# Performance work log

Measured on AMD Instinct MI355X. Metric: run time of the kernel, lower is better.

The kernel has to match this reference:

```python
import jax, jax.numpy as jnp
import numpy as np

K_MAX, K_MIN = 12.0, 1.0
TEMP = 1.0
STE_ALPHA = 12.0
EPS = 1e-8

DIM, HID, KHID, WHID = 512, 2048, 128, 128
B, N = 8, 1024


def setup_inputs() -> dict:
    key = jax.random.key(0)
    ks = jax.random.split(key, 13)
    def lin(k, fan_in, shape):
        bound = 1.0 / np.sqrt(fan_in)
        return jax.random.uniform(k, shape, jnp.float32, -bound, bound)
    return {
        "x": jax.random.normal(ks[0], (B, N, DIM), jnp.float32),
        "fc1_w": lin(ks[1], DIM, (HID, DIM)),
        "fc1_b": lin(ks[2], DIM, (HID,)),
        "fc2_w": lin(ks[3], HID, (DIM, HID)),
        "fc2_b": lin(ks[4], HID, (DIM,)),
        "k1_w": lin(ks[5], DIM, (KHID, DIM)),
        "k1_b": lin(ks[6], DIM, (KHID,)),
        "k2_w": lin(ks[7], KHID, (3, KHID)),
        "k2_b": lin(ks[8], KHID, (3,)),
        "w1_w": lin(ks[9], DIM, (WHID, DIM)),
        "w1_b": lin(ks[10], DIM, (WHID,)),
        "w2_w": lin(ks[11], WHID, (3, WHID)),
        "w2_b": lin(ks[12], WHID, (3,)),
    }


def adaptive_knn_aggregate(h, k_cont):
    # h: (B,N,C), k_cont: (B,) continuous k in [k_min, k_max]
    sim = jnp.einsum("bnc,bmc->bnm", h, h) / TEMP          # (B,N,N)
    order = jnp.argsort(-sim, axis=-1)                      # descending
    rank = jnp.argsort(order, axis=-1).astype(h.dtype)      # rank 0 = most similar
    # soft top-k gate (STE-style sigmoid around k_cont)
    gate = jax.nn.sigmoid(STE_ALPHA * (k_cont[:, None, None] - (rank + 0.5)))
    attn = jax.nn.softmax(sim, axis=-1) * gate
    attn = attn / (attn.sum(axis=-1, keepdims=True) + EPS)
    return jnp.einsum("bnm,bmc->bnc", attn, h)


def reference(x, fc1_w, fc1_b, fc2_w, fc2_b, k1_w, k1_b, k2_w, k2_b,
              w1_w, w1_b, w2_w, w2_b):
    pooled = x.mean(axis=1)                                 # (B,C)
    # adaptive k values net
    kh = jax.nn.relu(pooled @ k1_w.T + k1_b)
    ratio = jax.nn.sigmoid(kh @ k2_w.T + k2_b)              # (B,3)
    k_cont = K_MIN + ratio * (K_MAX - K_MIN)
    # adaptive branch weights net
    wh = jax.nn.relu(pooled @ w1_w.T + w1_b)
    w = jax.nn.softmax(wh @ w2_w.T + w2_b, axis=-1)         # (B,3)
    # MLP (dropout p=0 -> identity)
    h = jax.nn.relu(x @ fc1_w.T + fc1_b)
    h = h @ fc2_w.T + fc2_b                                 # (B,N,C)
    # three KNN aggregation branches blended by w
    y = sum(adaptive_knn_aggregate(h, k_cont[:, i]) * w[:, i, None, None]
            for i in range(3))
    return y
```

## Files before the change

### kernel.cpp

```cpp
#include <hip/hip_runtime.h>
#include <math.h>

#define DIM_ 512
#define HID_ 2048
#define B_ 8
#define N_ 1024
#define ROWS_ 8192
#define TOPK 16

typedef __attribute__((ext_vector_type(8))) short short8;
typedef __attribute__((ext_vector_type(4))) float float4v;

__device__ __forceinline__ float sigm(float x) { return 1.f / (1.f + __expf(-x)); }

__device__ __forceinline__ short f2bf(float f) {
    unsigned u = __float_as_uint(f);
    u += 0x7FFF + ((u >> 16) & 1);
    return (short)(u >> 16);
}

__device__ __forceinline__ float bf2f(unsigned short s) {
    return __uint_as_float((unsigned)s << 16);
}

__device__ __forceinline__ unsigned f2ord(float f) {
    unsigned u = __float_as_uint(f);
    return (u & 0x80000000u) ? ~u : (u | 0x80000000u);
}

__device__ __forceinline__ void gload16(const short* g, short* l) {
    __builtin_amdgcn_global_load_lds(
        (const __attribute__((address_space(1))) void*)g,
        (__attribute__((address_space(3))) void*)l, 16, 0, 0);
}

__global__ __launch_bounds__(256)
void cvt_w_kernel(const float* __restrict__ w1, const float* __restrict__ w2,
                  short* __restrict__ o1, short* __restrict__ o2) {
    const int i = blockIdx.x * 256 + threadIdx.x;
    const int n4 = HID_ * DIM_ / 4;
    const float* in = (i < n4) ? w1 : w2;
    short* out = (i < n4) ? o1 : o2;
    const int j = (i < n4) ? i : (i - n4);
    const float4 v = *(const float4*)(in + (long long)j * 4);
    short4 o;
    o.x = f2bf(v.x); o.y = f2bf(v.y); o.z = f2bf(v.z); o.w = f2bf(v.w);
    *(short4*)(out + (long long)j * 4) = o;
}

__global__ __launch_bounds__(512)
void pool_part_cvt_kernel(const float* __restrict__ x, float* __restrict__ part,
                          short* __restrict__ xb) {
    const int bx = blockIdx.x;
    const int b = bx >> 5, chunk = bx & 31;
    const int c = threadIdx.x;
    const long long base = ((long long)b * N_ + chunk * 32) * DIM_ + c;
    const float* xp = x + base;
    short* xo = xb + base;
    float s = 0.f;
    for (int n = 0; n < 32; ++n) {
        const float v = xp[(long long)n * DIM_];
        s += v;
        xo[(long long)n * DIM_] = f2bf(v);
    }
    part[(long long)bx * DIM_ + c] = s;
}

__global__ __launch_bounds__(512)
void pool_heads_kernel(const float* __restrict__ part,
                       const float* __restrict__ k1w, const float* __restrict__ k1b,
                       const float* __restrict__ k2w, const float* __restrict__ k2b,
                       const float* __restrict__ w1w, const float* __restrict__ w1b,
                       const float* __restrict__ w2w, const float* __restrict__ w2b,
                       float* __restrict__ kcont, float* __restrict__ wbr) {
    const int b = blockIdx.x;
    const int t = threadIdx.x;
    __shared__ float sp[DIM_];
    __shared__ float kh[128], wh[128];
    __shared__ float wraw[4];
    float s = 0.f;
    for (int g = 0; g < 32; ++g) s += part[((long long)b * 32 + g) * DIM_ + t];
    sp[t] = s * (1.f / 1024.f);
    __syncthreads();
    if (t < 128) {
        float ak = k1b[t], aw = w1b[t];
        for (int k = 0; k < DIM_; ++k) {
            const float pv = sp[k];
            ak = fmaf(pv, k1w[t * DIM_ + k], ak);
            aw = fmaf(pv, w1w[t * DIM_ + k], aw);
        }
        kh[t] = fmaxf(ak, 0.f);
        wh[t] = fmaxf(aw, 0.f);
    }
    __syncthreads();
    if (t < 3) {
        float rk = k2b[t], rw = w2b[t];
        for (int k = 0; k < 128; ++k) {
            rk = fmaf(kh[k], k2w[t * 128 + k], rk);
            rw = fmaf(wh[k], w2w[t * 128 + k], rw);
        }
        kcont[b * 3 + t] = 1.f + 11.f * sigm(rk);
        wraw[t] = rw;
    }
    __syncthreads();
    if (t == 0) {
        const float m = fmaxf(wraw[0], fmaxf(wraw[1], wraw[2]));
        const float e0 = __expf(wraw[0] - m), e1 = __expf(wraw[1] - m), e2 = __expf(wraw[2] - m);
        const float inv = 1.f / (e0 + e1 + e2);
        wbr[b * 3 + 0] = e0 * inv;
        wbr[b * 3 + 1] = e1 * inv;
        wbr[b * 3 + 2] = e2 * inv;
    }
}

template<int OUTMODE>
__global__ __launch_bounds__(256)
void gemm_mfma(const short* __restrict__ A, const short* __restrict__ Bm,
               const float* __restrict__ bias,
               float* __restrict__ outF, short* __restrict__ outB,
               int M, int N, int K, int lda, int ldb,
               long long sA, long long sB, long long sC) {
    const int bz = blockIdx.z;
    A  += (long long)bz * sA;
    Bm += (long long)bz * sB;

    __shared__ short As[128 * 64];
    __shared__ short Bs[128 * 64];

    const int tid = threadIdx.x;
    const int lane = tid & 63;
    const int wv = tid >> 6;
    const int m0 = blockIdx.y * 128;
    const int n0 = blockIdx.x * 128;

    const int lrow = lane >> 3;
    const int cg = (lane & 7) ^ lrow;

    const int ml = (wv & 1) * 64;
    const int nl = (wv >> 1) * 64;
    const int fr = lane & 15;
    const int kq = lane >> 4;

    float4v acc[4][4];
#pragma unroll
    for (int i = 0; i < 4; ++i)
#pragma unroll
        for (int j = 0; j < 4; ++j) acc[i][j] = (float4v){0.f, 0.f, 0.f, 0.f};

    for (int k0 = 0; k0 < K; k0 += 64) {
        __syncthreads();
#pragma unroll
        for (int i = 0; i < 4; ++i) {
            const int rloc = wv * 32 + i * 8 + lrow;
            gload16(A + (long long)(m0 + rloc) * lda + (k0 + cg * 8),
                    &As[(wv * 32 + i * 8) * 64]);
            gload16(Bm + (long long)(n0 + rloc) * ldb + (k0 + cg * 8),
                    &Bs[(wv * 32 + i * 8) * 64]);
        }
        __syncthreads();
#pragma unroll
        for (int ks = 0; ks < 2; ++ks) {
            const int c = ks * 4 + kq;
            short8 af[4], bfr[4];
#pragma unroll
            for (int i = 0; i < 4; ++i) {
                const int m = ml + i * 16 + fr;
                af[i] = *(const short8*)&As[m * 64 + ((c ^ (m & 7)) * 8)];
                const int n = nl + i * 16 + fr;
                bfr[i] = *(const short8*)&Bs[n * 64 + ((c ^ (n & 7)) * 8)];
            }
#pragma unroll
            for (int i = 0; i < 4; ++i)
#pragma unroll
                for (int j = 0; j < 4; ++j)
                    acc[i][j] = __builtin_amdgcn_mfma_f32_16x16x32_bf16(
                        af[i], bfr[j], acc[i][j], 0, 0, 0);
        }
    }

    const long long outOfs = (long long)bz * sC;
#pragma unroll
    for (int i = 0; i < 4; ++i) {
#pragma unroll
        for (int j = 0; j < 4; ++j) {
            const int ng = n0 + nl + j * 16 + fr;
            float bv = 0.f;
            if (OUTMODE != 2) bv = bias[ng];
#pragma unroll
            for (int r = 0; r < 4; ++r) {
                const int mg = m0 + ml + i * 16 + kq * 4 + r;
                float v = acc[i][j][r] + bv;
                if (OUTMODE == 0) v = fmaxf(v, 0.f);
                const long long idx = outOfs + (long long)mg * N + ng;
                if (OUTMODE == 2) outF[idx] = v;
                else              outB[idx] = f2bf(v);
            }
        }
    }
}

__global__ __launch_bounds__(256)
void combine_kernel(const float* __restrict__ p0, const float* __restrict__ p1,
                    const float* __restrict__ bias, short* __restrict__ out) {
    const int i = blockIdx.x * 256 + threadIdx.x;
    const long long o = (long long)i * 4;
    const float4 a = *(const float4*)(p0 + o);
    const float4 b = *(const float4*)(p1 + o);
    const int col = (int)(o & (DIM_ - 1));
    const float4 bs = *(const float4*)(bias + col);
    short4 r;
    r.x = f2bf(a.x + b.x + bs.x);
    r.y = f2bf(a.y + b.y + bs.y);
    r.z = f2bf(a.z + b.z + bs.z);
    r.w = f2bf(a.w + b.w + bs.w);
    *(short4*)(out + o) = r;
}

__global__ __launch_bounds__(256)
void topk_agg_kernel(const float* __restrict__ sim,
                     const float* __restrict__ kcont, const float* __restrict__ wbr,
                     const unsigned short* __restrict__ h, float* __restrict__ y) {
    const int wv = threadIdx.x >> 6;
    const int lane = threadIdx.x & 63;
    const int ll = lane & 15;
    const int row = blockIdx.x * 4 + wv;
    const int b = row >> 10;
    const float* srow = sim + (long long)row * N_;

    float f[16];
    const int base = lane * 16;
#pragma unroll
    for (int q = 0; q < 4; ++q) {
        const float4 v = *(const float4*)(srow + base + q * 4);
        f[q * 4 + 0] = v.x; f[q * 4 + 1] = v.y; f[q * 4 + 2] = v.z; f[q * 4 + 3] = v.w;
    }

    float lmax = f[0];
#pragma unroll
    for (int j = 1; j < 16; ++j) lmax = fmaxf(lmax, f[j]);
#pragma unroll
    for (int d = 32; d > 0; d >>= 1) lmax = fmaxf(lmax, __shfl_xor(lmax, d));
    const float maxv = lmax;

    float lsum = 0.f;
#pragma unroll
    for (int j = 0; j < 16; ++j) lsum += __expf(f[j] - maxv);
#pragma unroll
    for (int d = 32; d > 0; d >>= 1) lsum += __shfl_xor(lsum, d);
    const float invden = 1.f / lsum;

    unsigned key[16];
#pragma unroll
    for (int j = 0; j < 16; ++j)
        key[j] = (f2ord(f[j]) & 0xFFFFFC00u) | (unsigned)(1023 - (base + j));

#pragma unroll
    for (int k = 2; k <= 16; k <<= 1) {
#pragma unroll
        for (int j = k >> 1; j > 0; j >>= 1) {
#pragma unroll
            for (int i = 0; i < 16; ++i) {
                const int l = i ^ j;
                if (l > i) {
                    const bool desc = ((i & k) == 0);
                    const unsigned a = key[i], bk = key[l];
                    const unsigned hi = (a > bk) ? a : bk;
                    const unsigned lo = (a > bk) ? bk : a;
                    key[i] = desc ? hi : lo;
                    key[l] = desc ? lo : hi;
                }
            }
        }
    }

#pragma unroll
    for (int d = 1; d < 64; d <<= 1) {
        unsigned other[16];
#pragma unroll
        for (int i = 0; i < 16; ++i)
            other[i] = __shfl_xor(key[15 - i], d);
#pragma unroll
        for (int i = 0; i < 16; ++i)
            key[i] = (key[i] > other[i]) ? key[i] : other[i];
#pragma unroll
        for (int j = 8; j > 0; j >>= 1) {
#pragma unroll
            for (int i = 0; i < 16; ++i) {
                if ((i & j) == 0) {
                    const unsigned a = key[i], bk = key[i | j];
                    key[i]     = (a > bk) ? a : bk;
                    key[i | j] = (a > bk) ? bk : a;
                }
            }
        }
    }

    unsigned k32 = key[0];
#pragma unroll
    for (int j = 1; j < 16; ++j) k32 = (ll == j) ? key[j] : k32;
    const int myidx = 1023 - (int)(k32 & 1023u);
    const float myval = srow[myidx];

    unsigned long long kx = ((unsigned long long)f2ord(myval) << 32)
                          | (unsigned)(1023 - myidx);
#pragma unroll
    for (int k = 2; k <= 16; k <<= 1) {
#pragma unroll
        for (int d = k >> 1; d > 0; d >>= 1) {
            const unsigned long long other = __shfl_xor(kx, d);
            const bool keepMax = (((ll & k) != 0) == ((ll & d) != 0));
            const bool mineBig = (kx > other);
            kx = (keepMax == mineBig) ? kx : other;
        }
    }
    const unsigned sord = (unsigned)(kx >> 32);
    const unsigned su = (sord & 0x80000000u) ? (sord & 0x7FFFFFFFu) : ~sord;
    const float sval = __uint_as_float(su);
    const int sidx = 1023 - (int)(kx & 1023u);

    const float kc0 = kcont[b * 3 + 0], kc1 = kcont[b * 3 + 1], kc2 = kcont[b * 3 + 2];
    const float w0 = wbr[b * 3 + 0], w1 = wbr[b * 3 + 1], w2 = wbr[b * 3 + 2];

    const float p = __expf(sval - maxv) * invden;
    const float rr = (float)ll + 0.5f;
    const float g0 = sigm(12.f * (kc0 - rr));
    const float g1 = sigm(12.f * (kc1 - rr));
    const float g2 = sigm(12.f * (kc2 - rr));
    float s0 = p * g0, s1 = p * g1, s2 = p * g2;
#pragma unroll
    for (int d = 1; d < 16; d <<= 1) {
        s0 += __shfl_xor(s0, d);
        s1 += __shfl_xor(s1, d);
        s2 += __shfl_xor(s2, d);
    }
    const float f0 = w0 / (s0 + 1e-8f);
    const float f1 = w1 / (s1 + 1e-8f);
    const float f2 = w2 / (s2 + 1e-8f);
    const float mycoef = p * (f0 * g0 + f1 * g1 + f2 * g2);

    const int gbase = lane & 48;
    const unsigned short* hbase = h + (long long)b * (N_ * DIM_) + lane * 8;
    float acc[8] = {0.f, 0.f, 0.f, 0.f, 0.f, 0.f, 0.f, 0.f};
#pragma unroll
    for (int r = 0; r < 16; ++r) {
        const float coef = __shfl(mycoef, gbase | r);
        const int idx = __shfl(sidx, gbase | r);
        const ushort4 h0 = *(const ushort4*)(hbase + (long long)idx * DIM_);
        const ushort4 h1 = *(const ushort4*)(hbase + (long long)idx * DIM_ + 4);
        acc[0] = fmaf(coef, bf2f(h0.x), acc[0]);
        acc[1] = fmaf(coef, bf2f(h0.y), acc[1]);
        acc[2] = fmaf(coef, bf2f(h0.z), acc[2]);
        acc[3] = fmaf(coef, bf2f(h0.w), acc[3]);
        acc[4] = fmaf(coef, bf2f(h1.x), acc[4]);
        acc[5] = fmaf(coef, bf2f(h1.y), acc[5]);
        acc[6] = fmaf(coef, bf2f(h1.z), acc[6]);
        acc[7] = fmaf(coef, bf2f(h1.w), acc[7]);
    }
    float* yp = y + (long long)row * DIM_ + lane * 8;
    *(float4*)(yp + 0) = make_float4(acc[0], acc[1], acc[2], acc[3]);
    *(float4*)(yp + 4) = make_float4(acc[4], acc[5], acc[6], acc[7]);
}

extern "C" void kernel_launch(void* const* d_in, const int* in_sizes, int n_in,
                              void* d_out, int out_size, void* d_ws, size_t ws_size,
                              hipStream_t stream) {
    const float* x     = (const float*)d_in[0];
    const float* fc1_w = (const float*)d_in[1];
    const float* fc1_b = (const float*)d_in[2];
    const float* fc2_w = (const float*)d_in[3];
    const float* fc2_b = (const float*)d_in[4];
    const float* k1_w  = (const float*)d_in[5];
    const float* k1_b  = (const float*)d_in[6];
    const float* k2_w  = (const float*)d_in[7];
    const float* k2_b  = (const float*)d_in[8];
    const float* w1_w  = (const float*)d_in[9];
    const float* w1_b  = (const float*)d_in[10];
    const float* w2_w  = (const float*)d_in[11];
    const float* w2_b  = (const float*)d_in[12];

    char* ws = (char*)d_ws;
    short* h1b    = (short*)(ws + 0);
    float* simbuf = (float*)(ws + 0);
    short* xb     = (short*)(ws + 33554432);
    float* part0  = (float*)(ws + 33554432);
    float* part1  = (float*)(ws + 50331648);
    short* hb     = (short*)(ws + 67108864);
    short* w1b    = (short*)(ws + 75497472);
    short* w2b    = (short*)(ws + 77594624);
    float* ppart  = (float*)(ws + 79691776);
    float* kcont  = (float*)(ws + 80216064);
    float* wbr    = (float*)(ws + 80216192);

    float* y = (float*)d_out;

    cvt_w_kernel<<<dim3(2 * HID_ * DIM_ / 4 / 256), dim3(256), 0, stream>>>(fc1_w, fc2_w, w1b, w2b);
    pool_part_cvt_kernel<<<dim3(B_ * 32), dim3(512), 0, stream>>>(x, ppart, xb);
    pool_heads_kernel<<<dim3(B_), dim3(512), 0, stream>>>(ppart, k1_w, k1_b, k2_w, k2_b,
                                                          w1_w, w1_b, w2_w, w2_b, kcont, wbr);
    gemm_mfma<0><<<dim3(HID_ / 128, ROWS_ / 128, 1), dim3(256), 0, stream>>>(
        xb, w1b, fc1_b, nullptr, h1b, ROWS_, HID_, DIM_, DIM_, DIM_, 0, 0, 0);
    gemm_mfma<2><<<dim3(DIM_ / 128, ROWS_ / 128, 2), dim3(256), 0, stream>>>(
        h1b, w2b, nullptr, part0, nullptr, ROWS_, DIM_, HID_ / 2, HID_, HID_,
        (long long)(HID_ / 2), (long long)(HID_ / 2), (long long)ROWS_ * DIM_);
    combine_kernel<<<dim3(ROWS_ * DIM_ / 4 / 256), dim3(256), 0, stream>>>(part0, part1, fc2_b, hb);
    gemm_mfma<2><<<dim3(N_ / 128, N_ / 128, B_), dim3(256), 0, stream>>>(
        hb, hb, nullptr, simbuf, nullptr, N_, N_, DIM_, DIM_, DIM_,
        (long long)N_ * DIM_, (long long)N_ * DIM_, (long long)N_ * N_);
    topk_agg_kernel<<<dim3(ROWS_ / 4), dim3(256), 0, stream>>>(
        simbuf, kcont, wbr, (const unsigned short*)hb, y);
}
```

Measured before the change: 223.9 us.

## Switch GEMM to 32x32x16 MFMA and merge weight/input conversion kernels

The GEMM inner loop moves from 16x16x32 bf16 MFMA tiles (4x4 per wave) to 32x32x16 tiles (2x2 per wave), which halves the LDS fragment reads per MFMA and uses a larger matrix instruction. The epilogue row mapping is rewritten to match the 32x32 accumulator layout. Separately, the weight-conversion kernel and the pooling/x-conversion kernel are merged into one launch, removing one kernel launch. The larger accumulator layout changes the store pattern, so global write coalescing may differ.

```diff
diff --git a/kernel.cpp b/kernel.cpp
--- a/kernel.cpp
+++ b/kernel.cpp
@@ -9,7 +9,7 @@
 #define TOPK 16
 
 typedef __attribute__((ext_vector_type(8))) short short8;
-typedef __attribute__((ext_vector_type(4))) float float4v;
+typedef __attribute__((ext_vector_type(16))) float float16v;
 
 __device__ __forceinline__ float sigm(float x) { return 1.f / (1.f + __expf(-x)); }
 
@@ -34,36 +34,38 @@
         (__attribute__((address_space(3))) void*)l, 16, 0, 0);
 }
 
-__global__ __launch_bounds__(256)
-void cvt_w_kernel(const float* __restrict__ w1, const float* __restrict__ w2,
-                  short* __restrict__ o1, short* __restrict__ o2) {
-    const int i = blockIdx.x * 256 + threadIdx.x;
-    const int n4 = HID_ * DIM_ / 4;
-    const float* in = (i < n4) ? w1 : w2;
-    short* out = (i < n4) ? o1 : o2;
-    const int j = (i < n4) ? i : (i - n4);
-    const float4 v = *(const float4*)(in + (long long)j * 4);
-    short4 o;
-    o.x = f2bf(v.x); o.y = f2bf(v.y); o.z = f2bf(v.z); o.w = f2bf(v.w);
-    *(short4*)(out + (long long)j * 4) = o;
-}
-
 __global__ __launch_bounds__(512)
-void pool_part_cvt_kernel(const float* __restrict__ x, float* __restrict__ part,
-                          short* __restrict__ xb) {
+void prep_kernel(const float* __restrict__ x, float* __restrict__ part, short* __restrict__ xb,
+                 const float* __restrict__ w1, const float* __restrict__ w2,
+                 short* __restrict__ o1, short* __restrict__ o2) {
     const int bx = blockIdx.x;
-    const int b = bx >> 5, chunk = bx & 31;
-    const int c = threadIdx.x;
-    const long long base = ((long long)b * N_ + chunk * 32) * DIM_ + c;
-    const float* xp = x + base;
-    short* xo = xb + base;
-    float s = 0.f;
-    for (int n = 0; n < 32; ++n) {
-        const float v = xp[(long long)n * DIM_];
-        s += v;
-        xo[(long long)n * DIM_] = f2bf(v);
-    }
-    part[(long long)bx * DIM_ + c] = s;
+    if (bx < 256) {
+        const int b = bx >> 5, chunk = bx & 31;
+        const int c = threadIdx.x;
+        const long long base = ((long long)b * N_ + chunk * 32) * DIM_ + c;
+        const float* xp = x + base;
+        short* xo = xb + base;
+        float s = 0.f;
+        for (int n = 0; n < 32; ++n) {
+            const float v = xp[(long long)n * DIM_];
+            s += v;
+            xo[(long long)n * DIM_] = f2bf(v);
+        }
+        part[(long long)bx * DIM_ + c] = s;
+    } else {
+        const int n4 = HID_ * DIM_ / 4;
+        int i = (bx - 256) * 2048 + threadIdx.x;
+#pragma unroll
+        for (int t = 0; t < 4; ++t, i += 512) {
+            const float* in = (i < n4) ? w1 : w2;
+            short* out = (i < n4) ? o1 : o2;
+            const int j = (i < n4) ? i : (i - n4);
+            const float4 v = *(const float4*)(in + (long long)j * 4);
+            short4 o;
+            o.x = f2bf(v.x); o.y = f2bf(v.y); o.z = f2bf(v.z); o.w = f2bf(v.w);
+            *(short4*)(out + (long long)j * 4) = o;
+        }
+    }
 }
 
 __global__ __launch_bounds__(512)
@@ -138,14 +140,16 @@
 
     const int ml = (wv & 1) * 64;
     const int nl = (wv >> 1) * 64;
-    const int fr = lane & 15;
-    const int kq = lane >> 4;
-
-    float4v acc[4][4];
-#pragma unroll
-    for (int i = 0; i < 4; ++i)
-#pragma unroll
-        for (int j = 0; j < 4; ++j) acc[i][j] = (float4v){0.f, 0.f, 0.f, 0.f};
+    const int fr = lane & 31;
+    const int kh = lane >> 5;
+
+    float16v acc[2][2];
+#pragma unroll
+    for (int i = 0; i < 2; ++i)
+#pragma unroll
+        for (int j = 0; j < 2; ++j)
+#pragma unroll
+            for (int r = 0; r < 16; ++r) acc[i][j][r] = 0.f;
 
     for (int k0 = 0; k0 < K; k0 += 64) {
         __syncthreads();
@@ -159,36 +163,36 @@
         }
         __syncthreads();
 #pragma unroll
-        for (int ks = 0; ks < 2; ++ks) {
-            const int c = ks * 4 + kq;
-            short8 af[4], bfr[4];
-#pragma unroll
-            for (int i = 0; i < 4; ++i) {
-                const int m = ml + i * 16 + fr;
-                af[i] = *(const short8*)&As[m * 64 + ((c ^ (m & 7)) * 8)];
-                const int n = nl + i * 16 + fr;
-                bfr[i] = *(const short8*)&Bs[n * 64 + ((c ^ (n & 7)) * 8)];
+        for (int c = 0; c < 4; ++c) {
+            const int ch = c * 2 + kh;
+            short8 af[2], bfr[2];
+#pragma unroll
+            for (int i = 0; i < 2; ++i) {
+                const int m = ml + i * 32 + fr;
+                af[i] = *(const short8*)&As[m * 64 + ((ch ^ (m & 7)) * 8)];
+                const int n = nl + i * 32 + fr;
+                bfr[i] = *(const short8*)&Bs[n * 64 + ((ch ^ (n & 7)) * 8)];
             }
 #pragma unroll
-            for (int i = 0; i < 4; ++i)
-#pragma unroll
-                for (int j = 0; j < 4; ++j)
-                    acc[i][j] = __builtin_amdgcn_mfma_f32_16x16x32_bf16(
+            for (int i = 0; i < 2; ++i)
+#pragma unroll
+                for (int j = 0; j < 2; ++j)
+                    acc[i][j] = __builtin_amdgcn_mfma_f32_32x32x16_bf16(
                         af[i], bfr[j], acc[i][j], 0, 0, 0);
         }
     }
 
     const long long outOfs = (long long)bz * sC;
 #pragma unroll
-    for (int i = 0; i < 4; ++i) {
-#pragma unroll
-        for (int j = 0; j < 4; ++j) {
-            const int ng = n0 + nl + j * 16 + fr;
+    for (int i = 0; i < 2; ++i) {
+#pragma unroll
+        for (int j = 0; j < 2; ++j) {
+            const int ng = n0 + nl + j * 32 + fr;
             float bv = 0.f;
             if (OUTMODE != 2) bv = bias[ng];
 #pragma unroll
-            for (int r = 0; r < 4; ++r) {
-                const int mg = m0 + ml + i * 16 + kq * 4 + r;
+            for (int r = 0; r < 16; ++r) {
+                const int mg = m0 + ml + i * 32 + (r & 3) + 8 * (r >> 2) + 4 * kh;
                 float v = acc[i][j][r] + bv;
                 if (OUTMODE == 0) v = fmaxf(v, 0.f);
                 const long long idx = outOfs + (long long)mg * N + ng;
@@ -393,8 +397,7 @@
 
     float* y = (float*)d_out;
 
-    cvt_w_kernel<<<dim3(2 * HID_ * DIM_ / 4 / 256), dim3(256), 0, stream>>>(fc1_w, fc2_w, w1b, w2b);
-    pool_part_cvt_kernel<<<dim3(B_ * 32), dim3(512), 0, stream>>>(x, ppart, xb);
+    prep_kernel<<<dim3(512), dim3(512), 0, stream>>>(x, ppart, xb, fc1_w, fc2_w, w1b, w2b);
     pool_heads_kernel<<<dim3(B_), dim3(512), 0, stream>>>(ppart, k1_w, k1_b, k2_w, k2_b,
                                                           w1_w, w1_b, w2_w, w2_b, kcont, wbr);
     gemm_mfma<0><<<dim3(HID_ / 128, ROWS_ / 128, 1), dim3(256), 0, stream>>>(
```

New measurement: 221.2 us. Within noise of the previous version (-1.2%).
